# Performance work log

Measured on AMD Instinct MI355X. Metric: run time of the kernel, lower is better.

The kernel has to match this reference:

```python
import jax, jax.numpy as jnp
import numpy as np

B, N, DIN, DOUT = 8, 2048, 256, 256
ALPHA = 0.2  # leaky relu slope
EPS = 1e-6


def setup_inputs() -> dict:
    key = jax.random.key(0)
    k1, k2, k3, k4 = jax.random.split(key, 4)
    h = jax.random.normal(k1, (B, N, DIN), dtype=jnp.float32)
    adj = jax.random.uniform(k2, (B, N, N), dtype=jnp.float32)
    # xavier_uniform with gain=1.414
    gain = 1.414
    limW = gain * np.sqrt(6.0 / (DIN + DOUT))
    W = jax.random.uniform(k3, (DIN, DOUT), minval=-limW, maxval=limW, dtype=jnp.float32)
    lima = gain * np.sqrt(6.0 / (2 * DOUT + 1))
    a = jax.random.uniform(k4, (2 * DOUT, 1), minval=-lima, maxval=lima, dtype=jnp.float32)
    return {"h": h, "adj": adj, "W": W, "a": a}


def reference(h, adj, W, a):
    # Wh: [B, N, DOUT]
    Wh = jnp.einsum("bnd,df->bnf", h, W)
    # Split additive attention: cat([Wh_i, Wh_j]) @ a == Wh_i @ a1 + Wh_j @ a2
    a1 = a[:DOUT, 0]   # [DOUT]
    a2 = a[DOUT:, 0]   # [DOUT]
    s1 = Wh @ a1       # [B, N] score contribution of source node i
    s2 = Wh @ a2       # [B, N] score contribution of target node j
    e = s1[:, :, None] + s2[:, None, :]           # [B, N, N]
    e = jnp.where(e > 0, e, ALPHA * e)            # leaky relu
    e = e + jnp.log(adj + EPS)                    # soft adjacency mask
    alpha_w = jax.nn.softmax(e, axis=-1)          # [B, N, N]
    # dropout is identity in eval / deterministic reference
    h_prime = jnp.einsum("bij,bjf->bif", alpha_w, Wh)
    return h_prime
```

## Files before the change

kernel.cpp:

```cpp
#include <hip/hip_runtime.h>
#include <hip/hip_bf16.h>
#include <stdint.h>

#define ALPHA_ 0.2f
#define EPS_   1e-6f

typedef __attribute__((ext_vector_type(8))) short  short8;
typedef __attribute__((ext_vector_type(4))) float  float4v;

static __device__ __forceinline__ unsigned short f2bf(float x) {
    union { float f; unsigned int u; } c; c.f = x;
    return (unsigned short)((c.u + 0x7fffu + ((c.u >> 16) & 1u)) >> 16);
}

__global__ __launch_bounds__(256) void k_wt(const float* __restrict__ W,
                                            unsigned short* __restrict__ WTs) {
    const int g  = blockIdx.x * 256 + threadIdx.x;
    const int fb = g >> 9, kc = (g >> 6) & 7, l = g & 63;
    const int m = l & 15, quad = l >> 4;
    const int f = fb * 16 + m, d0 = kc * 32 + quad * 8;
    unsigned short v[8];
#pragma unroll
    for (int i = 0; i < 8; ++i) v[i] = f2bf(W[(d0 + i) * 256 + f]);
    uint4 o;
    o.x = (unsigned)v[0] | ((unsigned)v[1] << 16);
    o.y = (unsigned)v[2] | ((unsigned)v[3] << 16);
    o.z = (unsigned)v[4] | ((unsigned)v[5] << 16);
    o.w = (unsigned)v[6] | ((unsigned)v[7] << 16);
    *(uint4*)(WTs + (size_t)g * 8) = o;
}

__global__ __launch_bounds__(256) void k_wh(const float* __restrict__ h,
                                            const unsigned short* __restrict__ WTs,
                                            const float* __restrict__ a,
                                            unsigned short* __restrict__ WhS,
                                            float* __restrict__ s1g,
                                            float* __restrict__ s2g) {
    __shared__ __align__(16) unsigned short A_lds[32][264];
    __shared__ __align__(16) unsigned short T_lds[256][40];
    __shared__ float s1p[32], s2p[32];
    const int t    = threadIdx.x;
    const int lane = t & 63;
    const int wv   = t >> 6;
    const int m    = lane & 15;
    const int quad = lane >> 4;
    const int r0   = blockIdx.x * 32;
    const int b    = blockIdx.x >> 6;
    const int jc   = blockIdx.x & 63;
    const int j0   = r0 & 2047;

    if (t < 32) { s1p[t] = 0.f; s2p[t] = 0.f; }

#pragma unroll
    for (int k = 0; k < 8; ++k) {
        const int flat = t + k * 256;
        const int r  = flat >> 6;
        const int d4 = flat & 63;
        float4v hv = *(const float4v*)(h + (size_t)(r0 + r) * 256 + d4 * 4);
        uint2 pk;
        pk.x = (unsigned)f2bf(hv.x) | ((unsigned)f2bf(hv.y) << 16);
        pk.y = (unsigned)f2bf(hv.z) | ((unsigned)f2bf(hv.w) << 16);
        *(uint2*)&A_lds[r][d4 * 4] = pk;
    }
    __syncthreads();

    const int fbase = wv * 64;
    float4v acc[2][4];
#pragma unroll
    for (int it = 0; it < 2; ++it)
#pragma unroll
        for (int ft = 0; ft < 4; ++ft)
#pragma unroll
            for (int r = 0; r < 4; ++r) acc[it][ft][r] = 0.f;

    const unsigned short* wtb = WTs + (size_t)(wv * 4) * 4096 + lane * 8;

#pragma unroll
    for (int kc = 0; kc < 8; ++kc) {
        short8 af0 = *(const short8*)&A_lds[m][kc * 32 + quad * 8];
        short8 af1 = *(const short8*)&A_lds[16 + m][kc * 32 + quad * 8];
#pragma unroll
        for (int ft = 0; ft < 4; ++ft) {
            short8 bf = *(const short8*)(wtb + (size_t)ft * 4096 + kc * 512);
            acc[0][ft] = __builtin_amdgcn_mfma_f32_16x16x32_bf16(af0, bf, acc[0][ft], 0, 0, 0);
            acc[1][ft] = __builtin_amdgcn_mfma_f32_16x16x32_bf16(af1, bf, acc[1][ft], 0, 0, 0);
        }
    }

    float a1v[4], a2v[4];
#pragma unroll
    for (int ft = 0; ft < 4; ++ft) {
        a1v[ft] = a[fbase + ft * 16 + m];
        a2v[ft] = a[256 + fbase + ft * 16 + m];
    }
#pragma unroll
    for (int it = 0; it < 2; ++it) {
#pragma unroll
        for (int reg = 0; reg < 4; ++reg) {
            float v1 = 0.f, v2 = 0.f;
#pragma unroll
            for (int ft = 0; ft < 4; ++ft) {
                const float c = acc[it][ft][reg];
                v1 = fmaf(c, a1v[ft], v1);
                v2 = fmaf(c, a2v[ft], v2);
            }
            v1 += __shfl_xor(v1, 1); v2 += __shfl_xor(v2, 1);
            v1 += __shfl_xor(v1, 2); v2 += __shfl_xor(v2, 2);
            v1 += __shfl_xor(v1, 4); v2 += __shfl_xor(v2, 4);
            v1 += __shfl_xor(v1, 8); v2 += __shfl_xor(v2, 8);
            if (m == 0) {
                const int row = it * 16 + quad * 4 + reg;
                atomicAdd(&s1p[row], v1);
                atomicAdd(&s2p[row], v2);
            }
        }
    }

#pragma unroll
    for (int it = 0; it < 2; ++it)
#pragma unroll
        for (int ft = 0; ft < 4; ++ft)
#pragma unroll
            for (int reg = 0; reg < 4; ++reg)
                T_lds[fbase + ft * 16 + m][it * 16 + quad * 4 + reg] =
                    f2bf(acc[it][ft][reg]);

    __syncthreads();

#pragma unroll
    for (int e = 0; e < 4; ++e) {
        const int idx = e * 256 + t;
        const int fb = idx >> 6, l = idx & 63;
        uint4 v = *(const uint4*)&T_lds[fb * 16 + (l & 15)][(l >> 4) * 8];
        *(uint4*)(WhS + ((size_t)(b * 64 + jc) * 16 + fb) * 512 + l * 8) = v;
    }

    if (t < 32) {
        s1g[(size_t)b * 2048 + j0 + t] = s1p[t];
        s2g[(size_t)b * 2048 + j0 + t] = s2p[t];
    }
}

static __device__ __forceinline__ uint2 pquad(float4v av, float4v s2v,
                                              float s1, float& rs) {
    float e0 = s1 + s2v.x, e1 = s1 + s2v.y, e2 = s1 + s2v.z, e3 = s1 + s2v.w;
    e0 = fmaxf(e0, ALPHA_ * e0); e1 = fmaxf(e1, ALPHA_ * e1);
    e2 = fmaxf(e2, ALPHA_ * e2); e3 = fmaxf(e3, ALPHA_ * e3);
    const float p0 = (av.x + EPS_) * __expf(e0);
    const float p1 = (av.y + EPS_) * __expf(e1);
    const float p2 = (av.z + EPS_) * __expf(e2);
    const float p3 = (av.w + EPS_) * __expf(e3);
    rs += (p0 + p1) + (p2 + p3);
    uint2 r;
    r.x = (unsigned)f2bf(p0) | ((unsigned)f2bf(p1) << 16);
    r.y = (unsigned)f2bf(p2) | ((unsigned)f2bf(p3) << 16);
    return r;
}

__global__ __launch_bounds__(256, 4) void k_attn(const float* __restrict__ adj,
                                                 const unsigned short* __restrict__ WhS,
                                                 const float* __restrict__ s1g,
                                                 const float* __restrict__ s2g,
                                                 float* __restrict__ out) {
    __shared__ __align__(16) unsigned short pbuf[2][32][140];
    __shared__ float rsum_lds[32];

    const int t    = threadIdx.x;
    const int lane = t & 63;
    const int wv   = t >> 6;
    const int m    = lane & 15;
    const int quad = lane >> 4;
    const int blk  = blockIdx.x;
    const int b    = blk & 7;
    const int fh   = (blk >> 3) & 1;
    const int i0   = (blk >> 4) * 32;

    const int ip = t >> 3;
    const int jq = t & 7;

    const float* adjp = adj + (size_t)(b * 2048 + i0 + ip) * 2048 + jq * 4;
    const float* s2p  = s2g + (size_t)b * 2048 + jq * 4;
    const float  s1v  = s1g[(size_t)b * 2048 + i0 + ip];

    const int fbb = fh * 8 + wv * 2;
    const unsigned short* whs = WhS + (size_t)b * 64 * 16 * 512;

    float4v acc[2][2];
#pragma unroll
    for (int it = 0; it < 2; ++it)
#pragma unroll
        for (int ft = 0; ft < 2; ++ft)
#pragma unroll
            for (int r = 0; r < 4; ++r) acc[it][ft][r] = 0.f;

    float rs = 0.f;

    float4v adjv[4], s2v[4];
#pragma unroll
    for (int c = 0; c < 4; ++c) {
        adjv[c] = *(const float4v*)(adjp + c * 32);
        s2v[c]  = *(const float4v*)(s2p + c * 32);
    }

    for (int step = 0; step < 16; ++step) {
        const int cur = step & 1;

#pragma unroll
        for (int c = 0; c < 4; ++c) {
            uint2 pk = pquad(adjv[c], s2v[c], s1v, rs);
            *(uint2*)&pbuf[cur][ip][jq * 4 + c * 32] = pk;
        }

        const int ns = (step + 1) & 15;
#pragma unroll
        for (int c = 0; c < 4; ++c) {
            adjv[c] = *(const float4v*)(adjp + (size_t)ns * 128 + c * 32);
            s2v[c]  = *(const float4v*)(s2p + (size_t)ns * 128 + c * 32);
        }

        __syncthreads();

#pragma unroll
        for (int kc = 0; kc < 4; ++kc) {
            const unsigned short* bp =
                whs + ((size_t)((step * 4 + kc) * 16 + fbb)) * 512 + lane * 8;
            short8 bf0 = *(const short8*)bp;
            short8 bf1 = *(const short8*)(bp + 512);
            short8 af0 = *(const short8*)&pbuf[cur][m][kc * 32 + quad * 8];
            short8 af1 = *(const short8*)&pbuf[cur][16 + m][kc * 32 + quad * 8];
            acc[0][0] = __builtin_amdgcn_mfma_f32_16x16x32_bf16(af0, bf0, acc[0][0], 0, 0, 0);
            acc[0][1] = __builtin_amdgcn_mfma_f32_16x16x32_bf16(af0, bf1, acc[0][1], 0, 0, 0);
            acc[1][0] = __builtin_amdgcn_mfma_f32_16x16x32_bf16(af1, bf0, acc[1][0], 0, 0, 0);
            acc[1][1] = __builtin_amdgcn_mfma_f32_16x16x32_bf16(af1, bf1, acc[1][1], 0, 0, 0);
        }
    }

    rs += __shfl_xor(rs, 1);
    rs += __shfl_xor(rs, 2);
    rs += __shfl_xor(rs, 4);
    if (jq == 0) rsum_lds[ip] = rs;
    __syncthreads();

#pragma unroll
    for (int reg = 0; reg < 4; ++reg) {
        const int row  = quad * 4 + reg;
        const float i0v = 1.0f / rsum_lds[row];
        const float i1v = 1.0f / rsum_lds[16 + row];
#pragma unroll
        for (int ft = 0; ft < 2; ++ft) {
            const int f = fh * 128 + wv * 32 + ft * 16 + m;
            out[(size_t)(b * 2048 + i0 + row) * 256 + f]      = acc[0][ft][reg] * i0v;
            out[(size_t)(b * 2048 + i0 + 16 + row) * 256 + f] = acc[1][ft][reg] * i1v;
        }
    }
}

extern "C" void kernel_launch(void* const* d_in, const int* in_sizes, int n_in,
                              void* d_out, int out_size, void* d_ws, size_t ws_size,
                              hipStream_t stream) {
    const float* h   = (const float*)d_in[0];
    const float* adj = (const float*)d_in[1];
    const float* W   = (const float*)d_in[2];
    const float* a   = (const float*)d_in[3];
    float* out = (float*)d_out;

    unsigned short* WhS = (unsigned short*)d_ws;
    unsigned short* WTs = (unsigned short*)((char*)d_ws + 8388608);
    float*          s1  = (float*)((char*)d_ws + 8388608 + 131072);
    float*          s2  = s1 + 16384;

    k_wt  <<<dim3(32),   dim3(256), 0, stream>>>(W, WTs);
    k_wh  <<<dim3(512),  dim3(256), 0, stream>>>(h, WTs, a, WhS, s1, s2);
    k_attn<<<dim3(1024), dim3(256), 0, stream>>>(adj, WhS, s1, s2, out);
}
```

Before: 241.4 us.

## Stage s2 in LDS and prefetch Wh fragments before the barrier

Copies the per-batch s2 vector into shared memory once per block, so the attention loop no longer reloads it from global memory every step. The Wh B-fragments for all four k-chunks are now loaded at the top of each step, before the probability computation and barrier, to hide their global latency behind the exp work. The __syncthreads is replaced by an explicit lgkmcnt wait plus s_barrier, so outstanding global loads are not forced to drain at the barrier. This adds 8 KB of LDS and more live vector registers, which may lower occupancy under the (256,4) launch bounds.

```diff
diff --git a/kernel.cpp b/kernel.cpp
--- a/kernel.cpp
+++ b/kernel.cpp
@@ -163,6 +163,7 @@
                                                  const float* __restrict__ s2g,
                                                  float* __restrict__ out) {
     __shared__ __align__(16) unsigned short pbuf[2][32][140];
+    __shared__ __align__(16) float s2_lds[2048];
     __shared__ float rsum_lds[32];
 
     const int t    = threadIdx.x;
@@ -179,11 +180,16 @@
     const int jq = t & 7;
 
     const float* adjp = adj + (size_t)(b * 2048 + i0 + ip) * 2048 + jq * 4;
-    const float* s2p  = s2g + (size_t)b * 2048 + jq * 4;
     const float  s1v  = s1g[(size_t)b * 2048 + i0 + ip];
 
+    {
+        const float* s2src = s2g + (size_t)b * 2048;
+        *(float4v*)&s2_lds[t * 4]        = *(const float4v*)(s2src + t * 4);
+        *(float4v*)&s2_lds[1024 + t * 4] = *(const float4v*)(s2src + 1024 + t * 4);
+    }
+
     const int fbb = fh * 8 + wv * 2;
-    const unsigned short* whs = WhS + (size_t)b * 64 * 16 * 512;
+    const unsigned short* whs = WhS + (size_t)b * 64 * 16 * 512 + lane * 8;
 
     float4v acc[2][2];
 #pragma unroll
@@ -195,43 +201,47 @@
 
     float rs = 0.f;
 
-    float4v adjv[4], s2v[4];
-#pragma unroll
-    for (int c = 0; c < 4; ++c) {
-        adjv[c] = *(const float4v*)(adjp + c * 32);
-        s2v[c]  = *(const float4v*)(s2p + c * 32);
-    }
+    float4v adjv[4];
+#pragma unroll
+    for (int c = 0; c < 4; ++c) adjv[c] = *(const float4v*)(adjp + c * 32);
+
+    __syncthreads();
 
     for (int step = 0; step < 16; ++step) {
         const int cur = step & 1;
 
-#pragma unroll
-        for (int c = 0; c < 4; ++c) {
-            uint2 pk = pquad(adjv[c], s2v[c], s1v, rs);
-            *(uint2*)&pbuf[cur][ip][jq * 4 + c * 32] = pk;
-        }
-
-        const int ns = (step + 1) & 15;
-#pragma unroll
-        for (int c = 0; c < 4; ++c) {
-            adjv[c] = *(const float4v*)(adjp + (size_t)ns * 128 + c * 32);
-            s2v[c]  = *(const float4v*)(s2p + (size_t)ns * 128 + c * 32);
-        }
-
-        __syncthreads();
-
+        short8 breg[4][2];
 #pragma unroll
         for (int kc = 0; kc < 4; ++kc) {
             const unsigned short* bp =
-                whs + ((size_t)((step * 4 + kc) * 16 + fbb)) * 512 + lane * 8;
-            short8 bf0 = *(const short8*)bp;
-            short8 bf1 = *(const short8*)(bp + 512);
+                whs + (size_t)((step * 4 + kc) * 16 + fbb) * 512;
+            breg[kc][0] = *(const short8*)bp;
+            breg[kc][1] = *(const short8*)(bp + 512);
+        }
+
+#pragma unroll
+        for (int c = 0; c < 4; ++c) {
+            float4v s2v = *(const float4v*)&s2_lds[step * 128 + jq * 4 + c * 32];
+            uint2 pk = pquad(adjv[c], s2v, s1v, rs);
+            *(uint2*)&pbuf[cur][ip][jq * 4 + c * 32] = pk;
+        }
+
+        const int ns = (step + 1) & 15;
+#pragma unroll
+        for (int c = 0; c < 4; ++c)
+            adjv[c] = *(const float4v*)(adjp + (size_t)ns * 128 + c * 32);
+
+        asm volatile("s_waitcnt lgkmcnt(0)" ::: "memory");
+        __builtin_amdgcn_s_barrier();
+
+#pragma unroll
+        for (int kc = 0; kc < 4; ++kc) {
             short8 af0 = *(const short8*)&pbuf[cur][m][kc * 32 + quad * 8];
             short8 af1 = *(const short8*)&pbuf[cur][16 + m][kc * 32 + quad * 8];
-            acc[0][0] = __builtin_amdgcn_mfma_f32_16x16x32_bf16(af0, bf0, acc[0][0], 0, 0, 0);
-            acc[0][1] = __builtin_amdgcn_mfma_f32_16x16x32_bf16(af0, bf1, acc[0][1], 0, 0, 0);
-            acc[1][0] = __builtin_amdgcn_mfma_f32_16x16x32_bf16(af1, bf0, acc[1][0], 0, 0, 0);
-            acc[1][1] = __builtin_amdgcn_mfma_f32_16x16x32_bf16(af1, bf1, acc[1][1], 0, 0, 0);
+            acc[0][0] = __builtin_amdgcn_mfma_f32_16x16x32_bf16(af0, breg[kc][0], acc[0][0], 0, 0, 0);
+            acc[0][1] = __builtin_amdgcn_mfma_f32_16x16x32_bf16(af0, breg[kc][1], acc[0][1], 0, 0, 0);
+            acc[1][0] = __builtin_amdgcn_mfma_f32_16x16x32_bf16(af1, breg[kc][0], acc[1][0], 0, 0, 0);
+            acc[1][1] = __builtin_amdgcn_mfma_f32_16x16x32_bf16(af1, breg[kc][1], acc[1][1], 0, 0, 0);
         }
     }
 
```

Measured after the change: 245.1 us. Within noise of the previous version (+1.5%).

## Halve attention row tile, double grid, widen Wh block and use packed bf16 convert

Applied to the files above, without the earlier changes.

The attention kernel now processes 16 query rows per block instead of 32, doubling the grid to 2048 blocks and raising the occupancy hint to 8 blocks per CU, with each thread loading 8 contiguous adj values. The Wh projection kernel uses 512 threads so each wave covers 32 output features instead of 64. Probability-to-bf16 packing switches to the packed intrinsic. The goal is more waves in flight to hide adj streaming latency. In exchange, each block reuses the WhS B-fragments across half as many rows, so WhS is read twice as often from cache.

```diff
diff --git a/kernel.cpp b/kernel.cpp
--- a/kernel.cpp
+++ b/kernel.cpp
@@ -30,7 +30,7 @@
     *(uint4*)(WTs + (size_t)g * 8) = o;
 }
 
-__global__ __launch_bounds__(256) void k_wh(const float* __restrict__ h,
+__global__ __launch_bounds__(512) void k_wh(const float* __restrict__ h,
                                             const unsigned short* __restrict__ WTs,
                                             const float* __restrict__ a,
                                             unsigned short* __restrict__ WhS,
@@ -52,8 +52,8 @@
     if (t < 32) { s1p[t] = 0.f; s2p[t] = 0.f; }
 
 #pragma unroll
-    for (int k = 0; k < 8; ++k) {
-        const int flat = t + k * 256;
+    for (int k = 0; k < 4; ++k) {
+        const int flat = t + k * 512;
         const int r  = flat >> 6;
         const int d4 = flat & 63;
         float4v hv = *(const float4v*)(h + (size_t)(r0 + r) * 256 + d4 * 4);
@@ -64,32 +64,32 @@
     }
     __syncthreads();
 
-    const int fbase = wv * 64;
-    float4v acc[2][4];
+    const int fbase = wv * 32;
+    float4v acc[2][2];
 #pragma unroll
     for (int it = 0; it < 2; ++it)
 #pragma unroll
-        for (int ft = 0; ft < 4; ++ft)
+        for (int ft = 0; ft < 2; ++ft)
 #pragma unroll
             for (int r = 0; r < 4; ++r) acc[it][ft][r] = 0.f;
 
-    const unsigned short* wtb = WTs + (size_t)(wv * 4) * 4096 + lane * 8;
+    const unsigned short* wtb = WTs + (size_t)(wv * 2) * 4096 + lane * 8;
 
 #pragma unroll
     for (int kc = 0; kc < 8; ++kc) {
         short8 af0 = *(const short8*)&A_lds[m][kc * 32 + quad * 8];
         short8 af1 = *(const short8*)&A_lds[16 + m][kc * 32 + quad * 8];
 #pragma unroll
-        for (int ft = 0; ft < 4; ++ft) {
+        for (int ft = 0; ft < 2; ++ft) {
             short8 bf = *(const short8*)(wtb + (size_t)ft * 4096 + kc * 512);
             acc[0][ft] = __builtin_amdgcn_mfma_f32_16x16x32_bf16(af0, bf, acc[0][ft], 0, 0, 0);
             acc[1][ft] = __builtin_amdgcn_mfma_f32_16x16x32_bf16(af1, bf, acc[1][ft], 0, 0, 0);
         }
     }
 
-    float a1v[4], a2v[4];
-#pragma unroll
-    for (int ft = 0; ft < 4; ++ft) {
+    float a1v[2], a2v[2];
+#pragma unroll
+    for (int ft = 0; ft < 2; ++ft) {
         a1v[ft] = a[fbase + ft * 16 + m];
         a2v[ft] = a[256 + fbase + ft * 16 + m];
     }
@@ -99,7 +99,7 @@
         for (int reg = 0; reg < 4; ++reg) {
             float v1 = 0.f, v2 = 0.f;
 #pragma unroll
-            for (int ft = 0; ft < 4; ++ft) {
+            for (int ft = 0; ft < 2; ++ft) {
                 const float c = acc[it][ft][reg];
                 v1 = fmaf(c, a1v[ft], v1);
                 v2 = fmaf(c, a2v[ft], v2);
@@ -119,7 +119,7 @@
 #pragma unroll
     for (int it = 0; it < 2; ++it)
 #pragma unroll
-        for (int ft = 0; ft < 4; ++ft)
+        for (int ft = 0; ft < 2; ++ft)
 #pragma unroll
             for (int reg = 0; reg < 4; ++reg)
                 T_lds[fbase + ft * 16 + m][it * 16 + quad * 4 + reg] =
@@ -128,8 +128,8 @@
     __syncthreads();
 
 #pragma unroll
-    for (int e = 0; e < 4; ++e) {
-        const int idx = e * 256 + t;
+    for (int e = 0; e < 2; ++e) {
+        const int idx = e * 512 + t;
         const int fb = idx >> 6, l = idx & 63;
         uint4 v = *(const uint4*)&T_lds[fb * 16 + (l & 15)][(l >> 4) * 8];
         *(uint4*)(WhS + ((size_t)(b * 64 + jc) * 16 + fb) * 512 + l * 8) = v;
@@ -139,6 +139,13 @@
         s1g[(size_t)b * 2048 + j0 + t] = s1p[t];
         s2g[(size_t)b * 2048 + j0 + t] = s2p[t];
     }
+}
+
+static __device__ __forceinline__ unsigned pk2bf(float lo, float hi) {
+    float2 v; v.x = lo; v.y = hi;
+    union { __hip_bfloat162 h2; unsigned u; } cv;
+    cv.h2 = __float22bfloat162_rn(v);
+    return cv.u;
 }
 
 static __device__ __forceinline__ uint2 pquad(float4v av, float4v s2v,
@@ -152,18 +159,18 @@
     const float p3 = (av.w + EPS_) * __expf(e3);
     rs += (p0 + p1) + (p2 + p3);
     uint2 r;
-    r.x = (unsigned)f2bf(p0) | ((unsigned)f2bf(p1) << 16);
-    r.y = (unsigned)f2bf(p2) | ((unsigned)f2bf(p3) << 16);
+    r.x = pk2bf(p0, p1);
+    r.y = pk2bf(p2, p3);
     return r;
 }
 
-__global__ __launch_bounds__(256, 4) void k_attn(const float* __restrict__ adj,
+__global__ __launch_bounds__(256, 8) void k_attn(const float* __restrict__ adj,
                                                  const unsigned short* __restrict__ WhS,
                                                  const float* __restrict__ s1g,
                                                  const float* __restrict__ s2g,
                                                  float* __restrict__ out) {
-    __shared__ __align__(16) unsigned short pbuf[2][32][140];
-    __shared__ float rsum_lds[32];
+    __shared__ __align__(16) unsigned short pbuf[2][16][140];
+    __shared__ float rsum_lds[16];
 
     const int t    = threadIdx.x;
     const int lane = t & 63;
@@ -173,49 +180,47 @@
     const int blk  = blockIdx.x;
     const int b    = blk & 7;
     const int fh   = (blk >> 3) & 1;
-    const int i0   = (blk >> 4) * 32;
-
-    const int ip = t >> 3;
-    const int jq = t & 7;
-
-    const float* adjp = adj + (size_t)(b * 2048 + i0 + ip) * 2048 + jq * 4;
-    const float* s2p  = s2g + (size_t)b * 2048 + jq * 4;
+    const int i0   = (blk >> 4) * 16;
+
+    const int ip = t >> 4;
+    const int jq = t & 15;
+
+    const float* adjp = adj + (size_t)(b * 2048 + i0 + ip) * 2048 + jq * 8;
+    const float* s2p  = s2g + (size_t)b * 2048 + jq * 8;
     const float  s1v  = s1g[(size_t)b * 2048 + i0 + ip];
 
     const int fbb = fh * 8 + wv * 2;
     const unsigned short* whs = WhS + (size_t)b * 64 * 16 * 512;
 
-    float4v acc[2][2];
-#pragma unroll
-    for (int it = 0; it < 2; ++it)
-#pragma unroll
-        for (int ft = 0; ft < 2; ++ft)
-#pragma unroll
-            for (int r = 0; r < 4; ++r) acc[it][ft][r] = 0.f;
+    float4v acc[2];
+#pragma unroll
+    for (int ft = 0; ft < 2; ++ft)
+#pragma unroll
+        for (int r = 0; r < 4; ++r) acc[ft][r] = 0.f;
 
     float rs = 0.f;
 
-    float4v adjv[4], s2v[4];
-#pragma unroll
-    for (int c = 0; c < 4; ++c) {
-        adjv[c] = *(const float4v*)(adjp + c * 32);
-        s2v[c]  = *(const float4v*)(s2p + c * 32);
+    float4v adjv[2], s2v[2];
+#pragma unroll
+    for (int c = 0; c < 2; ++c) {
+        adjv[c] = *(const float4v*)(adjp + c * 4);
+        s2v[c]  = *(const float4v*)(s2p + c * 4);
     }
 
     for (int step = 0; step < 16; ++step) {
         const int cur = step & 1;
 
 #pragma unroll
-        for (int c = 0; c < 4; ++c) {
+        for (int c = 0; c < 2; ++c) {
             uint2 pk = pquad(adjv[c], s2v[c], s1v, rs);
-            *(uint2*)&pbuf[cur][ip][jq * 4 + c * 32] = pk;
+            *(uint2*)&pbuf[cur][ip][jq * 8 + c * 4] = pk;
         }
 
         const int ns = (step + 1) & 15;
 #pragma unroll
-        for (int c = 0; c < 4; ++c) {
-            adjv[c] = *(const float4v*)(adjp + (size_t)ns * 128 + c * 32);
-            s2v[c]  = *(const float4v*)(s2p + (size_t)ns * 128 + c * 32);
+        for (int c = 0; c < 2; ++c) {
+            adjv[c] = *(const float4v*)(adjp + (size_t)ns * 128 + c * 4);
+            s2v[c]  = *(const float4v*)(s2p + (size_t)ns * 128 + c * 4);
         }
 
         __syncthreads();
@@ -226,31 +231,27 @@
                 whs + ((size_t)((step * 4 + kc) * 16 + fbb)) * 512 + lane * 8;
             short8 bf0 = *(const short8*)bp;
             short8 bf1 = *(const short8*)(bp + 512);
-            short8 af0 = *(const short8*)&pbuf[cur][m][kc * 32 + quad * 8];
-            short8 af1 = *(const short8*)&pbuf[cur][16 + m][kc * 32 + quad * 8];
-            acc[0][0] = __builtin_amdgcn_mfma_f32_16x16x32_bf16(af0, bf0, acc[0][0], 0, 0, 0);
-            acc[0][1] = __builtin_amdgcn_mfma_f32_16x16x32_bf16(af0, bf1, acc[0][1], 0, 0, 0);
-            acc[1][0] = __builtin_amdgcn_mfma_f32_16x16x32_bf16(af1, bf0, acc[1][0], 0, 0, 0);
-            acc[1][1] = __builtin_amdgcn_mfma_f32_16x16x32_bf16(af1, bf1, acc[1][1], 0, 0, 0);
+            short8 af  = *(const short8*)&pbuf[cur][m][kc * 32 + quad * 8];
+            acc[0] = __builtin_amdgcn_mfma_f32_16x16x32_bf16(af, bf0, acc[0], 0, 0, 0);
+            acc[1] = __builtin_amdgcn_mfma_f32_16x16x32_bf16(af, bf1, acc[1], 0, 0, 0);
         }
     }
 
     rs += __shfl_xor(rs, 1);
     rs += __shfl_xor(rs, 2);
     rs += __shfl_xor(rs, 4);
+    rs += __shfl_xor(rs, 8);
     if (jq == 0) rsum_lds[ip] = rs;
     __syncthreads();
 
 #pragma unroll
     for (int reg = 0; reg < 4; ++reg) {
         const int row  = quad * 4 + reg;
-        const float i0v = 1.0f / rsum_lds[row];
-        const float i1v = 1.0f / rsum_lds[16 + row];
+        const float iv = 1.0f / rsum_lds[row];
 #pragma unroll
         for (int ft = 0; ft < 2; ++ft) {
             const int f = fh * 128 + wv * 32 + ft * 16 + m;
-            out[(size_t)(b * 2048 + i0 + row) * 256 + f]      = acc[0][ft][reg] * i0v;
-            out[(size_t)(b * 2048 + i0 + 16 + row) * 256 + f] = acc[1][ft][reg] * i1v;
+            out[(size_t)(b * 2048 + i0 + row) * 256 + f] = acc[ft][reg] * iv;
         }
     }
 }
@@ -270,6 +271,6 @@
     float*          s2  = s1 + 16384;
 
     k_wt  <<<dim3(32),   dim3(256), 0, stream>>>(W, WTs);
-    k_wh  <<<dim3(512),  dim3(256), 0, stream>>>(h, WTs, a, WhS, s1, s2);
-    k_attn<<<dim3(1024), dim3(256), 0, stream>>>(adj, WhS, s1, s2, out);
-}
+    k_wh  <<<dim3(512),  dim3(512), 0, stream>>>(h, WTs, a, WhS, s1, s2);
+    k_attn<<<dim3(2048), dim3(256), 0, stream>>>(adj, WhS, s1, s2, out);
+}
```

After: 267.9 us. 1.11x slower.
